# Performance work log

Measured on AMD Instinct MI355X. Metric: run time of the kernel, lower is better.

Reference implementation:

```python
import jax, jax.numpy as jnp
import numpy as np


def _morton_inverse_perm(L: int):
    """Return inv such that out_flat = x[..., inv] reproduces ret[i][j] = x[ij].

    i collects odd bits of ij, j collects even bits (Z-order / Morton decode).
    """
    S = int(np.sqrt(L))
    bit_l = L.bit_length()
    ij = np.arange(L, dtype=np.int64)
    i = np.zeros(L, dtype=np.int64)
    j = np.zeros(L, dtype=np.int64)
    for bit in range(bit_l):
        b = (ij >> bit) & 1
        if bit % 2 == 1:
            i += b << (bit // 2)
        else:
            j += b << (bit // 2)
    flat = i * S + j  # destination flat index for source position ij
    inv = np.empty(L, dtype=np.int64)
    inv[flat] = ij    # inverse permutation: gather form
    return inv, S


def setup_inputs() -> dict:
    key = jax.random.key(0)
    B, C, L = 8, 64, 65536  # 256x256 spatial map flattened in Morton order
    x = jax.random.normal(key, (B, C, L), dtype=jnp.float32)
    return {"x": x}


def reference(x) -> jnp.ndarray:
    B, C, L = x.shape
    inv, S = _morton_inverse_perm(L)  # data-independent, static under jit
    inv = jnp.asarray(inv)
    # single gather replaces the quadruple nested scalar-assignment loop
    out = jnp.take(x, inv, axis=2).reshape(B, C, S, S)
    return out
```

## Files before the change

### kernel.cpp

```cpp
#include <hip/hip_runtime.h>


__device__ __forceinline__ unsigned compact1by1(unsigned x) {
    x &= 0x55555555u;
    x = (x ^ (x >> 1)) & 0x33333333u;
    x = (x ^ (x >> 2)) & 0x0f0f0f0fu;
    x = (x ^ (x >> 4)) & 0x00ff00ffu;
    x = (x ^ (x >> 8)) & 0x0000ffffu;
    return x;
}

__global__ __launch_bounds__(256) void Morton_decode_69312182223578_kernel(
        const float* __restrict__ x, float* __restrict__ out) {
    const unsigned b    = blockIdx.x;
    const unsigned bc   = b >> 4;
    const unsigned tile = b & 15u;
    const unsigned ti   = tile >> 2;
    const unsigned tj   = tile & 3u;
    const unsigned tile_morton =
        (tj & 1u) | ((ti & 1u) << 1) | ((tj >> 1) << 2) | ((ti >> 1) << 3);

    const float4* __restrict__ src =
        (const float4*)(x + (size_t)bc * 65536u + ((size_t)tile_morton << 12));
    float* __restrict__ dst = out + (size_t)bc * 65536u;

#pragma unroll
    for (int k = 0; k < 4; ++k) {
        const unsigned q = (unsigned)k * 256u + threadIdx.x;
        const float4 v = src[q];
        const unsigned qj = compact1by1(q);
        const unsigned qi = compact1by1(q >> 1);
        const unsigned i = ti * 64u + 2u * qi;
        const unsigned j = tj * 64u + 2u * qj;
        float* p = dst + (size_t)i * 256u + j;
        *(float2*)p         = make_float2(v.x, v.y);
        *(float2*)(p + 256) = make_float2(v.z, v.w);
    }
}

extern "C" void kernel_launch(void* const* d_in, const int* in_sizes, int n_in,
                              void* d_out, int out_size, void* d_ws, size_t ws_size,
                              hipStream_t stream) {
    const float* x = (const float*)d_in[0];
    float* out = (float*)d_out;
    Morton_decode_69312182223578_kernel<<<8192, 256, 0, stream>>>(x, out);
}
```

Baseline: 230.0 us.

## Stage Morton tiles through swizzled LDS to emit full-row coalesced stores

Each block now loads 32KB chunks of the Morton-ordered input into shared memory, using an XOR swizzle to avoid bank conflicts. It then writes complete 256-float output row pairs with 16-byte vector stores, replacing the earlier scattered float2 stores. The grid shrinks to 1024 blocks, each looping over 4 tasks with barriers in between. This trades scattered global writes for LDS traffic, syncs and lower occupancy from 32KB of LDS per block.

New measurement: 236.3 us. 2.8% more time.

```diff
diff --git a/kernel.cpp b/kernel.cpp
--- a/kernel.cpp
+++ b/kernel.cpp
@@ -1,40 +1,55 @@
 #include <hip/hip_runtime.h>
 
 
-__device__ __forceinline__ unsigned compact1by1(unsigned x) {
-    x &= 0x55555555u;
-    x = (x ^ (x >> 1)) & 0x33333333u;
-    x = (x ^ (x >> 2)) & 0x0f0f0f0fu;
-    x = (x ^ (x >> 4)) & 0x00ff00ffu;
-    x = (x ^ (x >> 8)) & 0x0000ffffu;
-    return x;
+typedef float f32x4 __attribute__((ext_vector_type(4)));
+
+__device__ __forceinline__ unsigned swz(unsigned q) {
+    return q ^ ((q >> 4) & 1u) ^ (((q >> 6) & 1u) << 1);
 }
 
 __global__ __launch_bounds__(256) void Morton_decode_69312182223578_kernel(
         const float* __restrict__ x, float* __restrict__ out) {
-    const unsigned b    = blockIdx.x;
-    const unsigned bc   = b >> 4;
-    const unsigned tile = b & 15u;
-    const unsigned ti   = tile >> 2;
-    const unsigned tj   = tile & 3u;
-    const unsigned tile_morton =
-        (tj & 1u) | ((ti & 1u) << 1) | ((tj >> 1) << 2) | ((ti >> 1) << 3);
+    __shared__ f32x4 lds[2048];
 
-    const float4* __restrict__ src =
-        (const float4*)(x + (size_t)bc * 65536u + ((size_t)tile_morton << 12));
-    float* __restrict__ dst = out + (size_t)bc * 65536u;
+    const unsigned t = threadIdx.x;
+    const unsigned w = t >> 6;
+    const unsigned l = t & 63u;
 
-#pragma unroll
-    for (int k = 0; k < 4; ++k) {
-        const unsigned q = (unsigned)k * 256u + threadIdx.x;
-        const float4 v = src[q];
-        const unsigned qj = compact1by1(q);
-        const unsigned qi = compact1by1(q >> 1);
-        const unsigned i = ti * 64u + 2u * qi;
-        const unsigned j = tj * 64u + 2u * qj;
-        float* p = dst + (size_t)i * 256u + j;
-        *(float2*)p         = make_float2(v.x, v.y);
-        *(float2*)(p + 256) = make_float2(v.z, v.w);
+    const unsigned task0 = blockIdx.x * 4u;
+    for (unsigned task = task0; task < task0 + 4u; ++task) {
+        const unsigned img = task >> 3;
+        const unsigned s   = task & 7u;
+        const size_t img_base = (size_t)img << 16;
+        const size_t src_base = img_base + ((size_t)(s & 1u) << 11)
+                                         + ((size_t)((s >> 1) & 1u) << 13)
+                                         + ((size_t)(s >> 2) << 15);
+        const size_t dst_base = img_base + ((size_t)s << 13);
+
+        #pragma unroll
+        for (unsigned k = 0; k < 8; ++k) {
+            const unsigned qw = k * 256u + t;
+            const unsigned gq = (qw & 511u) | ((qw & 512u) << 1) | ((qw & 1024u) << 2);
+            const f32x4 v = *(const f32x4*)(x + src_base + ((size_t)gq << 2));
+            lds[swz(qw)] = v;
+        }
+        __syncthreads();
+
+        #pragma unroll
+        for (unsigned k = 0; k < 4; ++k) {
+            const unsigned m = w * 4u + k;
+            const unsigned K = (m & 1u) | ((l & 1u) << 1)
+                             | (((m >> 1) & 1u) << 2) | (((l >> 1) & 1u) << 3)
+                             | (((m >> 2) & 1u) << 4) | (((l >> 2) & 1u) << 5)
+                             | ((m >> 3) << 6) | ((l >> 3) << 7);
+            const f32x4 qA = lds[swz(2u * K)];
+            const f32x4 qB = lds[swz(2u * K + 1u)];
+            const f32x4 top = {qA.x, qA.y, qB.x, qB.y};
+            const f32x4 bot = {qA.z, qA.w, qB.z, qB.w};
+            float* p = out + dst_base + ((size_t)(2u * m) << 8) + 4u * l;
+            *(f32x4*)p         = top;
+            *(f32x4*)(p + 256) = bot;
+        }
+        __syncthreads();
     }
 }
 
@@ -43,5 +58,5 @@
                               hipStream_t stream) {
     const float* x = (const float*)d_in[0];
     float* out = (float*)d_out;
-    Morton_decode_69312182223578_kernel<<<8192, 256, 0, stream>>>(x, out);
+    Morton_decode_69312182223578_kernel<<<1024, 256, 0, stream>>>(x, out);
 }
```
